# Optimization experiments

Hardware: AMD Instinct MI355X
Metric: run time of the kernel (lower is better)

## Reference

```python
import jax, jax.numpy as jnp
import numpy as np

B, S, D, H = 4, 2048, 1024, 16
HD = D // H  # head dim = 64


def setup_inputs() -> dict:
    key = jax.random.key(0)
    ks = jax.random.split(key, 10)
    sd = 1.0 / np.sqrt(D)
    return {
        "x": jax.random.normal(ks[0], (B, S, D), jnp.float32),
        "Wq": jax.random.normal(ks[1], (D, D), jnp.float32) * sd,
        "Wk": jax.random.normal(ks[2], (D, D), jnp.float32) * sd,
        "Wv": jax.random.normal(ks[3], (D, D), jnp.float32) * sd,
        "in_w": jax.random.normal(ks[4], (3 * D, D), jnp.float32) * sd,
        "in_b": jax.random.normal(ks[5], (3 * D,), jnp.float32) * 0.01,
        "out_w": jax.random.normal(ks[6], (D, D), jnp.float32) * sd,
        "out_b": jax.random.normal(ks[7], (D,), jnp.float32) * 0.01,
        "proj_w": jax.random.normal(ks[8], (D, D), jnp.float32) * sd,
        "proj_b": jax.random.normal(ks[9], (D,), jnp.float32) * 0.01,
    }


def _attn_block(x, Wq, Wk, Wv, in_w, in_b, out_w, out_b, proj_w, proj_b):
    b, s, d = x.shape
    # redundant pre-projections (bias-free)
    q = jnp.einsum('bsd,ed->bse', x, Wq)
    k = jnp.einsum('bsd,ed->bse', x, Wk)
    v = jnp.einsum('bsd,ed->bse', x, Wv)
    # MultiheadAttention internal in-projection (with bias)
    wq, wk, wv = in_w[:d], in_w[d:2 * d], in_w[2 * d:]
    bq, bk, bv = in_b[:d], in_b[d:2 * d], in_b[2 * d:]
    Q = jnp.einsum('bse,fe->bsf', q, wq) + bq
    K = jnp.einsum('bse,fe->bsf', k, wk) + bk
    V = jnp.einsum('bse,fe->bsf', v, wv) + bv
    # split heads -> [b, h, s, hd]
    Q = Q.reshape(b, s, H, HD).transpose(0, 2, 1, 3)
    K = K.reshape(b, s, H, HD).transpose(0, 2, 1, 3)
    V = V.reshape(b, s, H, HD).transpose(0, 2, 1, 3)
    scale = 1.0 / np.sqrt(HD)
    scores = jnp.einsum('bhqd,bhkd->bhqk', Q * scale, K)
    # FAITHFUL quirk: float tril mask (ones / zeros) is ADDED to scores,
    # exactly as torch does with a float attn_mask (not a -inf causal mask).
    mask = jnp.tril(jnp.ones((s, s), scores.dtype))
    scores = scores + mask
    A = jax.nn.softmax(scores, axis=-1)
    ctx = jnp.einsum('bhqk,bhkd->bhqd', A, V)
    ctx = ctx.transpose(0, 2, 1, 3).reshape(b, s, d)
    attn = jnp.einsum('bse,fe->bsf', ctx, out_w) + out_b  # out_proj
    out = jnp.einsum('bse,fe->bsf', attn, proj_w) + proj_b  # self.project
    return x + out


def reference(x, Wq, Wk, Wv, in_w, in_b, out_w, out_b, proj_w, proj_b):
    return _attn_block(x, Wq, Wk, Wv, in_w, in_b, out_w, out_b, proj_w, proj_b)
```

## Files before the change

### kernel.cpp

```cpp
#include <hip/hip_runtime.h>
#include <stdint.h>

typedef unsigned short u16;
typedef __attribute__((ext_vector_type(8))) short bfx8;
typedef __attribute__((ext_vector_type(4))) float fx4;
typedef __attribute__((ext_vector_type(2))) unsigned int uint32x2;

static __device__ __forceinline__ u16 f2b(float f) {
  union { float f; uint32_t u; } v; v.f = f;
  uint32_t r = v.u + 0x7fffu + ((v.u >> 16) & 1u);
  return (u16)(r >> 16);
}

static __device__ __forceinline__ uint32_t cvtpk(float lo, float hi) {
  uint32_t r;
  asm("v_cvt_pk_bf16_f32 %0, %1, %2" : "=v"(r) : "v"(lo), "v"(hi));
  return r;
}

static __device__ __forceinline__ void gload16(const void* g, void* lds) {
  __builtin_amdgcn_global_load_lds((const __attribute__((address_space(1))) uint32_t*)g,
                                   (__attribute__((address_space(3))) uint32_t*)lds,
                                   16, 0, 0);
}

__global__ __launch_bounds__(256) void f32_to_bf16_k(const float* __restrict__ in,
                                                     u16* __restrict__ out, int n) {
  int i = (blockIdx.x * 256 + threadIdx.x) * 8;
  if (i >= n) return;
  float4 a = *(const float4*)(in + i);
  float4 b = *(const float4*)(in + i + 4);
  bfx8 o;
  o[0]=(short)f2b(a.x); o[1]=(short)f2b(a.y); o[2]=(short)f2b(a.z); o[3]=(short)f2b(a.w);
  o[4]=(short)f2b(b.x); o[5]=(short)f2b(b.y); o[6]=(short)f2b(b.z); o[7]=(short)f2b(b.w);
  *(bfx8*)(out + i) = o;
}

struct TransArgs { const float* in[4]; u16* out[4]; };
__global__ __launch_bounds__(256) void transpose4_k(TransArgs ta) {
  const float* in = ta.in[blockIdx.z];
  u16* out = ta.out[blockIdx.z];
  __shared__ u16 t[64][65];
  const int bx = blockIdx.x * 64, by = blockIdx.y * 64;
  const int tid = threadIdx.x;
#pragma unroll
  for (int i = 0; i < 16; ++i) {
    int idx = tid + i * 256; int r = idx >> 6, c = idx & 63;
    t[c][r] = f2b(in[(size_t)(by + r) * 1024 + bx + c]);
  }
  __syncthreads();
#pragma unroll
  for (int i = 0; i < 16; ++i) {
    int idx = tid + i * 256; int r = idx >> 6, c = idx & 63;
    out[(size_t)(bx + r) * 1024 + by + c] = t[r][c];
  }
}

__global__ __launch_bounds__(256) void make_b2_k(const float* __restrict__ pw,
                                                 const float* __restrict__ ob,
                                                 const float* __restrict__ pb,
                                                 float* __restrict__ b2) {
  const int f = blockIdx.x, tid = threadIdx.x;
  float s = 0.f;
  for (int e = tid; e < 1024; e += 256) s += pw[(size_t)f * 1024 + e] * ob[e];
#pragma unroll
  for (int d = 1; d < 64; d <<= 1) s += __shfl_xor(s, d);
  __shared__ float red[4];
  if ((tid & 63) == 0) red[tid >> 6] = s;
  __syncthreads();
  if (tid == 0) b2[f] = red[0] + red[1] + red[2] + red[3] + pb[f];
}

static __device__ __forceinline__ void gemm_core(const u16* __restrict__ A,
                                                 const u16* __restrict__ Bt,
                                                 int K, int bm, int bn,
                                                 u16* As, u16* Bs, fx4 (&acc)[4][4]) {
  const int tid = threadIdx.x, w = tid >> 6, l = tid & 63, lm = l & 15, lk = l >> 4;
  const int wm = w >> 1, wn = w & 1;
  const int nkt = K >> 6;
  for (int kt = 0; kt < nkt; ++kt) {
#pragma unroll
    for (int i = 0; i < 4; ++i) {
      int off = i * 4096 + w * 1024;
      int loff = off + l * 16;
      int row = loff >> 7, cb = loff & 127;
      gload16((const char*)A + ((size_t)(bm * 128 + row) * K + kt * 64) * 2 + cb,
              (char*)As + off);
      gload16((const char*)Bt + ((size_t)(bn * 128 + row) * K + kt * 64) * 2 + cb,
              (char*)Bs + off);
    }
    __syncthreads();
#pragma unroll
    for (int kk = 0; kk < 2; ++kk) {
      bfx8 a[4], b[4];
#pragma unroll
      for (int mi = 0; mi < 4; ++mi)
        a[mi] = *(const bfx8*)((const char*)As + (wm * 64 + mi * 16 + lm) * 128 + lk * 16 + kk * 64);
#pragma unroll
      for (int nj = 0; nj < 4; ++nj)
        b[nj] = *(const bfx8*)((const char*)Bs + (wn * 64 + nj * 16 + lm) * 128 + lk * 16 + kk * 64);
#pragma unroll
      for (int mi = 0; mi < 4; ++mi)
#pragma unroll
        for (int nj = 0; nj < 4; ++nj)
          acc[mi][nj] = __builtin_amdgcn_mfma_f32_16x16x32_bf16(a[mi], b[nj], acc[mi][nj], 0, 0, 0);
    }
    __syncthreads();
  }
}

struct CombArgs { const u16* A[4]; const u16* Bt[4]; u16* C[4]; };
__global__ __launch_bounds__(256) void gemm_combine_k(CombArgs ca) {
  const int z = blockIdx.z;
  __shared__ u16 As[8192], Bs[8192];
  fx4 acc[4][4];
#pragma unroll
  for (int mi = 0; mi < 4; ++mi)
#pragma unroll
    for (int nj = 0; nj < 4; ++nj) acc[mi][nj] = 0.f;
  gemm_core(ca.A[z], ca.Bt[z], 1024, blockIdx.x, blockIdx.y, As, Bs, acc);
  const int tid = threadIdx.x, w = tid >> 6, l = tid & 63, lm = l & 15, lk = l >> 4;
  const int wm = w >> 1, wn = w & 1;
  u16* C = ca.C[z];
#pragma unroll
  for (int mi = 0; mi < 4; ++mi)
#pragma unroll
    for (int nj = 0; nj < 4; ++nj)
#pragma unroll
      for (int r = 0; r < 4; ++r) {
        int m = blockIdx.x * 128 + wm * 64 + mi * 16 + lk * 4 + r;
        int n = blockIdx.y * 128 + wn * 64 + nj * 16 + lm;
        C[(size_t)m * 1024 + n] = f2b(acc[mi][nj][r]);
      }
}

__global__ __launch_bounds__(256) void gemm_qkv_k(const u16* __restrict__ xb,
                                                  const u16* __restrict__ Wc,
                                                  const float* __restrict__ bias,
                                                  u16* __restrict__ Qh, u16* __restrict__ Kh,
                                                  u16* __restrict__ Vh) {
  __shared__ u16 As[8192], Bs[8192];
  fx4 acc[4][4];
#pragma unroll
  for (int mi = 0; mi < 4; ++mi)
#pragma unroll
    for (int nj = 0; nj < 4; ++nj) acc[mi][nj] = 0.f;
  gemm_core(xb, Wc, 1024, blockIdx.x, blockIdx.y, As, Bs, acc);
  const int tid = threadIdx.x, w = tid >> 6, l = tid & 63, lm = l & 15, lk = l >> 4;
  const int wm = w >> 1, wn = w & 1;
  const int t = (blockIdx.y * 128) >> 10;
  u16* dst = (t == 0) ? Qh : ((t == 1) ? Kh : Vh);
#pragma unroll
  for (int mi = 0; mi < 4; ++mi)
#pragma unroll
    for (int nj = 0; nj < 4; ++nj)
#pragma unroll
      for (int r = 0; r < 4; ++r) {
        int m = blockIdx.x * 128 + wm * 64 + mi * 16 + lk * 4 + r;
        int n = blockIdx.y * 128 + wn * 64 + nj * 16 + lm;
        float v = acc[mi][nj][r] + bias[n];
        int f = n & 1023, h = f >> 6, hd = f & 63, b = m >> 11, s = m & 2047;
        size_t hb = ((size_t)(b * 16 + h)) * 131072;
        size_t idx;
        if (t == 2) {
          int sl = s & 63, st = s >> 6;
          idx = hb + (size_t)st * 4096 +
                (size_t)((sl >> 2) * 256 + (hd >> 4) * 64 + (sl & 3) * 16 + (hd & 15));
        } else if (t == 1) {
          idx = hb + (size_t)s * 64 + (hd ^ ((s & 7) << 3));
        } else {
          idx = hb + (size_t)s * 64 + hd;
        }
        dst[idx] = f2b(v);
      }
}

__global__ __launch_bounds__(256) void gemm_final_k(const u16* __restrict__ ctx,
                                                    const u16* __restrict__ W2,
                                                    const float* __restrict__ b2,
                                                    const float* __restrict__ x,
                                                    float* __restrict__ out) {
  __shared__ u16 As[8192], Bs[8192];
  fx4 acc[4][4];
#pragma unroll
  for (int mi = 0; mi < 4; ++mi)
#pragma unroll
    for (int nj = 0; nj < 4; ++nj) acc[mi][nj] = 0.f;
  gemm_core(ctx, W2, 1024, blockIdx.x, blockIdx.y, As, Bs, acc);
  const int tid = threadIdx.x, w = tid >> 6, l = tid & 63, lm = l & 15, lk = l >> 4;
  const int wm = w >> 1, wn = w & 1;
#pragma unroll
  for (int mi = 0; mi < 4; ++mi)
#pragma unroll
    for (int nj = 0; nj < 4; ++nj)
#pragma unroll
      for (int r = 0; r < 4; ++r) {
        int m = blockIdx.x * 128 + wm * 64 + mi * 16 + lk * 4 + r;
        int n = blockIdx.y * 128 + wn * 64 + nj * 16 + lm;
        size_t idx = (size_t)m * 1024 + n;
        out[idx] = acc[mi][nj][r] + b2[n] + x[idx];
      }
}

#define TRRD(d, IMM) asm volatile("ds_read_b64_tr_b16 %0, %1 offset:" IMM : "=v"(d) : "v"(va))

__global__ __launch_bounds__(256) void attn_k(const u16* __restrict__ Qh,
                                              const u16* __restrict__ Kh,
                                              const u16* __restrict__ Vh,
                                              u16* __restrict__ ctx) {
  const int bh = blockIdx.y, qt = blockIdx.x;
  const int tid = threadIdx.x, w = tid >> 6, l = tid & 63, lm = l & 15, lk = l >> 4;
  __shared__ __align__(16) u16 Ks[2][4096];
  __shared__ __align__(16) u16 Vs[2][4096];
  __shared__ __align__(16) u16 Pl[4][1024];

  const size_t base = (size_t)bh * 131072;
  bfx8 qf[2];
  {
    const u16* qp = Qh + base + (size_t)(qt * 64 + w * 16 + lm) * 64;
    qf[0] = *(const bfx8*)(qp + lk * 8);
    qf[1] = *(const bfx8*)(qp + lk * 8 + 32);
  }
  float m_run = -INFINITY, l_part = 0.f;
  fx4 accO[4];
#pragma unroll
  for (int nj = 0; nj < 4; ++nj) accO[nj] = 0.f;

  const char* Kg = (const char*)(Kh + base);
  const char* Vg = (const char*)(Vh + base);
  const int o0 = w * 1024 + l * 16, o1 = o0 + 4096;

  const int swz = (lm & 7) << 4;
  const uint32_t vs_base =
      (uint32_t)(uintptr_t)(__attribute__((address_space(3))) char*)&Vs[0][0];
  const uint32_t vtrb = vs_base + (uint32_t)(lk * 1024 + lm * 8);

  gload16(Kg + o0, (char*)Ks[0] + o0);
  gload16(Kg + o1, (char*)Ks[0] + o1);
  gload16(Vg + o0, (char*)Vs[0] + o0);
  gload16(Vg + o1, (char*)Vs[0] + o1);
  __syncthreads();

  const int qg = qt * 64 + w * 16 + lm;
  int cur = 0;
  for (int kt = 0; kt < 32; ++kt) {
    if (kt < 31) {
      int nb = cur ^ 1;
      const char* kg = Kg + (kt + 1) * 8192;
      const char* vg = Vg + (kt + 1) * 8192;
      gload16(kg + o0, (char*)Ks[nb] + o0);
      gload16(kg + o1, (char*)Ks[nb] + o1);
      gload16(vg + o0, (char*)Vs[nb] + o0);
      gload16(vg + o1, (char*)Vs[nb] + o1);
    }
    const char* Kc = (const char*)Ks[cur];
    fx4 s[4];
#pragma unroll
    for (int nj = 0; nj < 4; ++nj) s[nj] = 0.f;
#pragma unroll
    for (int kk = 0; kk < 2; ++kk)
#pragma unroll
      for (int nj = 0; nj < 4; ++nj) {
        bfx8 kf = *(const bfx8*)(Kc + nj * 2048 + lm * 128 +
                                 (((kk * 4 + lk) ^ (lm & 7)) << 4));
        s[nj] = __builtin_amdgcn_mfma_f32_16x16x32_bf16(kf, qf[kk], s[nj], 0, 0, 0);
      }
    if (kt < qt) {
#pragma unroll
      for (int nj = 0; nj < 4; ++nj)
#pragma unroll
        for (int r = 0; r < 4; ++r) s[nj][r] = fmaf(s[nj][r], 0.125f, 1.0f);
    } else if (kt > qt) {
#pragma unroll
      for (int nj = 0; nj < 4; ++nj)
#pragma unroll
        for (int r = 0; r < 4; ++r) s[nj][r] *= 0.125f;
    } else {
#pragma unroll
      for (int nj = 0; nj < 4; ++nj)
#pragma unroll
        for (int r = 0; r < 4; ++r) {
          int key = kt * 64 + nj * 16 + lk * 4 + r;
          s[nj][r] = s[nj][r] * 0.125f + ((key <= qg) ? 1.0f : 0.0f);
        }
    }
    float mx = fmaxf(fmaxf(fmaxf(s[0][0], s[0][1]), fmaxf(s[0][2], s[0][3])),
                     fmaxf(fmaxf(s[1][0], s[1][1]), fmaxf(s[1][2], s[1][3])));
    mx = fmaxf(mx, fmaxf(fmaxf(fmaxf(s[2][0], s[2][1]), fmaxf(s[2][2], s[2][3])),
                         fmaxf(fmaxf(s[3][0], s[3][1]), fmaxf(s[3][2], s[3][3]))));
    if (!__all(mx <= m_run + 8.0f)) {
      mx = fmaxf(mx, __shfl_xor(mx, 16));
      mx = fmaxf(mx, __shfl_xor(mx, 32));
      float mn = fmaxf(m_run, mx);
      float corr = __expf(m_run - mn);
      m_run = mn;
      l_part *= corr;
#pragma unroll
      for (int r = 0; r < 4; ++r) {
        float cr = __shfl(corr, (l & 48) | (lk * 4 + r));
#pragma unroll
        for (int nj = 0; nj < 4; ++nj) accO[nj][r] *= cr;
      }
    }
    float lsum = 0.f;
#pragma unroll
    for (int nj = 0; nj < 4; ++nj)
#pragma unroll
      for (int r = 0; r < 4; ++r) {
        float p = __expf(s[nj][r] - m_run);
        s[nj][r] = p;
        lsum += p;
      }
    l_part += lsum;
#pragma unroll
    for (int nj = 0; nj < 4; ++nj) {
      uint32x2 pw;
      pw[0] = cvtpk(s[nj][0], s[nj][1]);
      pw[1] = cvtpk(s[nj][2], s[nj][3]);
      *(uint32x2*)((char*)Pl[w] + ((lm * 128 + nj * 32 + lk * 8) ^ swz)) = pw;
    }
    uint32x2 tr[2][4][2];
    uint32_t va = vtrb + (uint32_t)(cur * 8192);
    TRRD(tr[0][0][0], "0");    TRRD(tr[0][0][1], "512");
    TRRD(tr[0][1][0], "128");  TRRD(tr[0][1][1], "640");
    TRRD(tr[0][2][0], "256");  TRRD(tr[0][2][1], "768");
    TRRD(tr[0][3][0], "384");  TRRD(tr[0][3][1], "896");
    TRRD(tr[1][0][0], "4096"); TRRD(tr[1][0][1], "4608");
    TRRD(tr[1][1][0], "4224"); TRRD(tr[1][1][1], "4736");
    TRRD(tr[1][2][0], "4352"); TRRD(tr[1][2][1], "4864");
    TRRD(tr[1][3][0], "4480"); TRRD(tr[1][3][1], "4992");
    asm volatile("s_waitcnt lgkmcnt(0)" ::: "memory");
    __builtin_amdgcn_sched_barrier(0);
#pragma unroll
    for (int kk = 0; kk < 2; ++kk) {
      bfx8 pf = *(const bfx8*)((char*)Pl[w] + ((lm * 128 + kk * 64 + lk * 16) ^ swz));
#pragma unroll
      for (int nj = 0; nj < 4; ++nj) {
        union { uint32x2 u2[2]; bfx8 v; } u;
        u.u2[0] = tr[kk][nj][0];
        u.u2[1] = tr[kk][nj][1];
        accO[nj] = __builtin_amdgcn_mfma_f32_16x16x32_bf16(pf, u.v, accO[nj], 0, 0, 0);
      }
    }
    __syncthreads();
    cur ^= 1;
  }

  float lt = l_part;
  lt += __shfl_xor(lt, 16);
  lt += __shfl_xor(lt, 32);
  const int b = bh >> 4, h = bh & 15;
#pragma unroll
  for (int r = 0; r < 4; ++r) {
    float li = __shfl(lt, (l & 48) | (lk * 4 + r));
    float inv = 1.0f / li;
    int q = qt * 64 + w * 16 + lk * 4 + r;
#pragma unroll
    for (int nj = 0; nj < 4; ++nj)
      ctx[((size_t)b * 2048 + q) * 1024 + h * 64 + nj * 16 + lm] = f2b(accO[nj][r] * inv);
  }
}

extern "C" void kernel_launch(void* const* d_in, const int* in_sizes, int n_in,
                              void* d_out, int out_size, void* d_ws, size_t ws_size,
                              hipStream_t stream) {
  (void)in_sizes; (void)n_in; (void)out_size; (void)ws_size;
  const float* x      = (const float*)d_in[0];
  const float* Wq     = (const float*)d_in[1];
  const float* Wk     = (const float*)d_in[2];
  const float* Wv     = (const float*)d_in[3];
  const float* in_w   = (const float*)d_in[4];
  const float* in_b   = (const float*)d_in[5];
  const float* out_w  = (const float*)d_in[6];
  const float* out_b  = (const float*)d_in[7];
  const float* proj_w = (const float*)d_in[8];
  const float* proj_b = (const float*)d_in[9];
  float* out = (float*)d_out;

  char* ws = (char*)d_ws;
  const size_t MB = 1ull << 20;
  u16* xb   = (u16*)(ws);
  u16* ctx  = xb;
  u16* Qh   = (u16*)(ws + 16 * MB);
  u16* Kh   = (u16*)(ws + 32 * MB);
  u16* Vh   = (u16*)(ws + 48 * MB);
  u16* inwb = Kh;
  u16* tmpT = Vh;
  u16* pwb  = (u16*)(ws + 48 * MB + 8 * MB);
  u16* Wc   = (u16*)(ws + 64 * MB);
  u16* W2   = (u16*)(ws + 70 * MB);
  float* b2 = (float*)(ws + 72 * MB);

  f32_to_bf16_k<<<4096, 256, 0, stream>>>(x, xb, 8388608);
  f32_to_bf16_k<<<1536, 256, 0, stream>>>(in_w, inwb, 3145728);
  f32_to_bf16_k<<<512, 256, 0, stream>>>(proj_w, pwb, 1048576);

  TransArgs ta;
  ta.in[0] = Wq; ta.in[1] = Wk; ta.in[2] = Wv; ta.in[3] = out_w;
  for (int z = 0; z < 4; ++z) ta.out[z] = tmpT + (size_t)z * 1048576;
  transpose4_k<<<dim3(16, 16, 4), 256, 0, stream>>>(ta);

  CombArgs ca;
  ca.A[0] = inwb; ca.A[1] = inwb + 1048576; ca.A[2] = inwb + 2097152; ca.A[3] = pwb;
  for (int z = 0; z < 4; ++z) ca.Bt[z] = tmpT + (size_t)z * 1048576;
  ca.C[0] = Wc; ca.C[1] = Wc + 1048576; ca.C[2] = Wc + 2097152; ca.C[3] = W2;
  gemm_combine_k<<<dim3(8, 8, 4), 256, 0, stream>>>(ca);

  make_b2_k<<<1024, 256, 0, stream>>>(proj_w, out_b, proj_b, b2);

  gemm_qkv_k<<<dim3(64, 24), 256, 0, stream>>>(xb, Wc, in_b, Qh, Kh, Vh);
  attn_k<<<dim3(32, 64), 256, 0, stream>>>(Qh, Kh, Vh, ctx);
  gemm_final_k<<<dim3(64, 8), 256, 0, stream>>>(ctx, W2, b2, x, out);
}
```

Measured before the change: 308.3 us.

## Process two query tiles per attention block and use native exp2 softmax

Each attention workgroup now handles 128 query rows (two 64-row groups) against the same K/V tiles, so every K/V load and V transpose read from LDS serves twice as many queries and the grid is halved. Scores are pre-scaled by log2(e) and exponentiated with the raw v_exp_f32 instruction in place of __expf, with the mask bias and rescale threshold adjusted to match. This costs more registers per thread (two sets of accumulators and scores) and 1024 workgroups instead of 2048, which may reduce occupancy.

```diff
diff --git a/kernel.cpp b/kernel.cpp
--- a/kernel.cpp
+++ b/kernel.cpp
@@ -15,6 +15,12 @@
 static __device__ __forceinline__ uint32_t cvtpk(float lo, float hi) {
   uint32_t r;
   asm("v_cvt_pk_bf16_f32 %0, %1, %2" : "=v"(r) : "v"(lo), "v"(hi));
+  return r;
+}
+
+static __device__ __forceinline__ float ex2(float x) {
+  float r;
+  asm("v_exp_f32 %0, %1" : "=v"(r) : "v"(x));
   return r;
 }
 
@@ -214,17 +220,25 @@
   __shared__ __align__(16) u16 Vs[2][4096];
   __shared__ __align__(16) u16 Pl[4][1024];
 
+  const float SC = 0.18033688011112042f;
+  const float MA = 1.4426950408889634f;
+  const float THR = 11.541560327111708f;
+
   const size_t base = (size_t)bh * 131072;
-  bfx8 qf[2];
-  {
-    const u16* qp = Qh + base + (size_t)(qt * 64 + w * 16 + lm) * 64;
-    qf[0] = *(const bfx8*)(qp + lk * 8);
-    qf[1] = *(const bfx8*)(qp + lk * 8 + 32);
-  }
-  float m_run = -INFINITY, l_part = 0.f;
-  fx4 accO[4];
-#pragma unroll
-  for (int nj = 0; nj < 4; ++nj) accO[nj] = 0.f;
+  bfx8 qf[2][2];
+#pragma unroll
+  for (int g = 0; g < 2; ++g) {
+    const u16* qp = Qh + base + (size_t)(qt * 128 + g * 64 + w * 16 + lm) * 64;
+    qf[g][0] = *(const bfx8*)(qp + lk * 8);
+    qf[g][1] = *(const bfx8*)(qp + lk * 8 + 32);
+  }
+  float m_run[2] = {-INFINITY, -INFINITY};
+  float l_part[2] = {0.f, 0.f};
+  fx4 accO[2][4];
+#pragma unroll
+  for (int g = 0; g < 2; ++g)
+#pragma unroll
+    for (int nj = 0; nj < 4; ++nj) accO[g][nj] = 0.f;
 
   const char* Kg = (const char*)(Kh + base);
   const char* Vg = (const char*)(Vh + base);
@@ -241,7 +255,6 @@
   gload16(Vg + o1, (char*)Vs[0] + o1);
   __syncthreads();
 
-  const int qg = qt * 64 + w * 16 + lm;
   int cur = 0;
   for (int kt = 0; kt < 32; ++kt) {
     if (kt < 31) {
@@ -254,69 +267,81 @@
       gload16(vg + o1, (char*)Vs[nb] + o1);
     }
     const char* Kc = (const char*)Ks[cur];
-    fx4 s[4];
-#pragma unroll
-    for (int nj = 0; nj < 4; ++nj) s[nj] = 0.f;
-#pragma unroll
-    for (int kk = 0; kk < 2; ++kk)
-#pragma unroll
-      for (int nj = 0; nj < 4; ++nj) {
-        bfx8 kf = *(const bfx8*)(Kc + nj * 2048 + lm * 128 +
-                                 (((kk * 4 + lk) ^ (lm & 7)) << 4));
-        s[nj] = __builtin_amdgcn_mfma_f32_16x16x32_bf16(kf, qf[kk], s[nj], 0, 0, 0);
-      }
-    if (kt < qt) {
+    fx4 s[2][4];
+#pragma unroll
+    for (int g = 0; g < 2; ++g)
+#pragma unroll
+      for (int nj = 0; nj < 4; ++nj) s[g][nj] = 0.f;
+#pragma unroll
+    for (int kk = 0; kk < 2; ++kk) {
+      bfx8 kf[4];
 #pragma unroll
       for (int nj = 0; nj < 4; ++nj)
-#pragma unroll
-        for (int r = 0; r < 4; ++r) s[nj][r] = fmaf(s[nj][r], 0.125f, 1.0f);
-    } else if (kt > qt) {
+        kf[nj] = *(const bfx8*)(Kc + nj * 2048 + lm * 128 +
+                                (((kk * 4 + lk) ^ (lm & 7)) << 4));
+#pragma unroll
+      for (int g = 0; g < 2; ++g)
+#pragma unroll
+        for (int nj = 0; nj < 4; ++nj)
+          s[g][nj] = __builtin_amdgcn_mfma_f32_16x16x32_bf16(kf[nj], qf[g][kk], s[g][nj], 0, 0, 0);
+    }
+#pragma unroll
+    for (int g = 0; g < 2; ++g) {
+      const int dk = kt - 2 * qt - g;
+      if (dk < 0) {
+#pragma unroll
+        for (int nj = 0; nj < 4; ++nj)
+#pragma unroll
+          for (int r = 0; r < 4; ++r) s[g][nj][r] = fmaf(s[g][nj][r], SC, MA);
+      } else if (dk > 0) {
+#pragma unroll
+        for (int nj = 0; nj < 4; ++nj)
+#pragma unroll
+          for (int r = 0; r < 4; ++r) s[g][nj][r] *= SC;
+      } else {
+        const int qg = qt * 128 + g * 64 + w * 16 + lm;
+#pragma unroll
+        for (int nj = 0; nj < 4; ++nj)
+#pragma unroll
+          for (int r = 0; r < 4; ++r) {
+            int key = kt * 64 + nj * 16 + lk * 4 + r;
+            s[g][nj][r] = s[g][nj][r] * SC + ((key <= qg) ? MA : 0.0f);
+          }
+      }
+      float mx = fmaxf(fmaxf(fmaxf(s[g][0][0], s[g][0][1]), fmaxf(s[g][0][2], s[g][0][3])),
+                       fmaxf(fmaxf(s[g][1][0], s[g][1][1]), fmaxf(s[g][1][2], s[g][1][3])));
+      mx = fmaxf(mx, fmaxf(fmaxf(fmaxf(s[g][2][0], s[g][2][1]), fmaxf(s[g][2][2], s[g][2][3])),
+                           fmaxf(fmaxf(s[g][3][0], s[g][3][1]), fmaxf(s[g][3][2], s[g][3][3]))));
+      if (!__all(mx <= m_run[g] + THR)) {
+        mx = fmaxf(mx, __shfl_xor(mx, 16));
+        mx = fmaxf(mx, __shfl_xor(mx, 32));
+        float mn = fmaxf(m_run[g], mx);
+        float corr = ex2(m_run[g] - mn);
+        m_run[g] = mn;
+        l_part[g] *= corr;
+#pragma unroll
+        for (int r = 0; r < 4; ++r) {
+          float cr = __shfl(corr, (l & 48) | (lk * 4 + r));
+#pragma unroll
+          for (int nj = 0; nj < 4; ++nj) accO[g][nj][r] *= cr;
+        }
+      }
+      float lsum = 0.f;
 #pragma unroll
       for (int nj = 0; nj < 4; ++nj)
 #pragma unroll
-        for (int r = 0; r < 4; ++r) s[nj][r] *= 0.125f;
-    } else {
-#pragma unroll
-      for (int nj = 0; nj < 4; ++nj)
-#pragma unroll
         for (int r = 0; r < 4; ++r) {
-          int key = kt * 64 + nj * 16 + lk * 4 + r;
-          s[nj][r] = s[nj][r] * 0.125f + ((key <= qg) ? 1.0f : 0.0f);
+          float p = ex2(s[g][nj][r] - m_run[g]);
+          s[g][nj][r] = p;
+          lsum += p;
         }
-    }
-    float mx = fmaxf(fmaxf(fmaxf(s[0][0], s[0][1]), fmaxf(s[0][2], s[0][3])),
-                     fmaxf(fmaxf(s[1][0], s[1][1]), fmaxf(s[1][2], s[1][3])));
-    mx = fmaxf(mx, fmaxf(fmaxf(fmaxf(s[2][0], s[2][1]), fmaxf(s[2][2], s[2][3])),
-                         fmaxf(fmaxf(s[3][0], s[3][1]), fmaxf(s[3][2], s[3][3]))));
-    if (!__all(mx <= m_run + 8.0f)) {
-      mx = fmaxf(mx, __shfl_xor(mx, 16));
-      mx = fmaxf(mx, __shfl_xor(mx, 32));
-      float mn = fmaxf(m_run, mx);
-      float corr = __expf(m_run - mn);
-      m_run = mn;
-      l_part *= corr;
-#pragma unroll
-      for (int r = 0; r < 4; ++r) {
-        float cr = __shfl(corr, (l & 48) | (lk * 4 + r));
-#pragma unroll
-        for (int nj = 0; nj < 4; ++nj) accO[nj][r] *= cr;
-      }
-    }
-    float lsum = 0.f;
-#pragma unroll
-    for (int nj = 0; nj < 4; ++nj)
-#pragma unroll
-      for (int r = 0; r < 4; ++r) {
-        float p = __expf(s[nj][r] - m_run);
-        s[nj][r] = p;
-        lsum += p;
-      }
-    l_part += lsum;
+      l_part[g] += lsum;
+    }
 #pragma unroll
     for (int nj = 0; nj < 4; ++nj) {
       uint32x2 pw;
-      pw[0] = cvtpk(s[nj][0], s[nj][1]);
-      pw[1] = cvtpk(s[nj][2], s[nj][3]);
+      pw[0] = cvtpk(s[0][nj][0], s[0][nj][1]);
+      pw[1] = cvtpk(s[0][nj][2], s[0][nj][3]);
       *(uint32x2*)((char*)Pl[w] + ((lm * 128 + nj * 32 + lk * 8) ^ swz)) = pw;
     }
     uint32x2 tr[2][4][2];
@@ -339,25 +364,46 @@
         union { uint32x2 u2[2]; bfx8 v; } u;
         u.u2[0] = tr[kk][nj][0];
         u.u2[1] = tr[kk][nj][1];
-        accO[nj] = __builtin_amdgcn_mfma_f32_16x16x32_bf16(pf, u.v, accO[nj], 0, 0, 0);
+        accO[0][nj] = __builtin_amdgcn_mfma_f32_16x16x32_bf16(pf, u.v, accO[0][nj], 0, 0, 0);
+      }
+    }
+#pragma unroll
+    for (int nj = 0; nj < 4; ++nj) {
+      uint32x2 pw;
+      pw[0] = cvtpk(s[1][nj][0], s[1][nj][1]);
+      pw[1] = cvtpk(s[1][nj][2], s[1][nj][3]);
+      *(uint32x2*)((char*)Pl[w] + ((lm * 128 + nj * 32 + lk * 8) ^ swz)) = pw;
+    }
+#pragma unroll
+    for (int kk = 0; kk < 2; ++kk) {
+      bfx8 pf = *(const bfx8*)((char*)Pl[w] + ((lm * 128 + kk * 64 + lk * 16) ^ swz));
+#pragma unroll
+      for (int nj = 0; nj < 4; ++nj) {
+        union { uint32x2 u2[2]; bfx8 v; } u;
+        u.u2[0] = tr[kk][nj][0];
+        u.u2[1] = tr[kk][nj][1];
+        accO[1][nj] = __builtin_amdgcn_mfma_f32_16x16x32_bf16(pf, u.v, accO[1][nj], 0, 0, 0);
       }
     }
     __syncthreads();
     cur ^= 1;
   }
 
-  float lt = l_part;
-  lt += __shfl_xor(lt, 16);
-  lt += __shfl_xor(lt, 32);
   const int b = bh >> 4, h = bh & 15;
 #pragma unroll
-  for (int r = 0; r < 4; ++r) {
-    float li = __shfl(lt, (l & 48) | (lk * 4 + r));
-    float inv = 1.0f / li;
-    int q = qt * 64 + w * 16 + lk * 4 + r;
-#pragma unroll
-    for (int nj = 0; nj < 4; ++nj)
-      ctx[((size_t)b * 2048 + q) * 1024 + h * 64 + nj * 16 + lm] = f2b(accO[nj][r] * inv);
+  for (int g = 0; g < 2; ++g) {
+    float lt = l_part[g];
+    lt += __shfl_xor(lt, 16);
+    lt += __shfl_xor(lt, 32);
+#pragma unroll
+    for (int r = 0; r < 4; ++r) {
+      float li = __shfl(lt, (l & 48) | (lk * 4 + r));
+      float inv = 1.0f / li;
+      int q = qt * 128 + g * 64 + w * 16 + lk * 4 + r;
+#pragma unroll
+      for (int nj = 0; nj < 4; ++nj)
+        ctx[((size_t)b * 2048 + q) * 1024 + h * 64 + nj * 16 + lm] = f2b(accO[g][nj][r] * inv);
+    }
   }
 }
 
@@ -409,6 +455,6 @@
   make_b2_k<<<1024, 256, 0, stream>>>(proj_w, out_b, proj_b, b2);
 
   gemm_qkv_k<<<dim3(64, 24), 256, 0, stream>>>(xb, Wc, in_b, Qh, Kh, Vh);
-  attn_k<<<dim3(32, 64), 256, 0, stream>>>(Qh, Kh, Vh, ctx);
+  attn_k<<<dim3(16, 64), 256, 0, stream>>>(Qh, Kh, Vh, ctx);
   gemm_final_k<<<dim3(64, 8), 256, 0, stream>>>(ctx, W2, b2, x, out);
 }
```

New measurement: 299.3 us. 2.9% less time.
